# Optimization experiments

Hardware: AMD Instinct MI355X
Metric: run time of the kernel (lower is better)

## Reference

```python
import jax, jax.numpy as jnp
import numpy as np
from jax import lax

B, S, CIN, COUT, K = 32, 2048, 256, 256, 16


def setup_inputs() -> dict:
    key = jax.random.key(0)
    k1, k2, k3, k4 = jax.random.split(key, 4)
    x = jax.random.normal(k1, (B, S, CIN), dtype=jnp.float32)
    w_real = jax.random.normal(k2, (COUT, CIN, K), dtype=jnp.float32) * 0.1
    w_imag = jax.random.normal(k3, (COUT, CIN, K), dtype=jnp.float32) * 0.1
    phases = jax.random.normal(k4, (K,), dtype=jnp.float32) * 0.1
    return {"x": x, "w_real": w_real, "w_imag": w_imag, "phases": phases}


def reference(x, w_real, w_imag, phases):
    # out[b,t,o] = Re( sum_{k,i} x[b,t+k,i] * exp(1j*phases[k]) * (w_real + 1j*w_imag)[o,i,k] )
    # x is real, so this equals a real valid conv1d with effective kernel:
    #   w_eff[o,i,k] = cos(phases[k]) * w_real[o,i,k] - sin(phases[k]) * w_imag[o,i,k]
    w_eff = jnp.cos(phases)[None, None, :] * w_real - jnp.sin(phases)[None, None, :] * w_imag
    # conv expects NCH / OIH layouts
    y = lax.conv_general_dilated(
        jnp.transpose(x, (0, 2, 1)),  # [B, CIN, S]
        w_eff,                         # [COUT, CIN, K]
        window_strides=(1,),
        padding="VALID",
        dimension_numbers=("NCH", "OIH", "NCH"),
    )
    return jnp.transpose(y, (0, 2, 1))  # [B, S-K+1, COUT]
```

## Files before the change

### kernel.cpp

```cpp
#include <hip/hip_runtime.h>
#include <math.h>

#define B_    32
#define S_    2048
#define CIN_  256
#define COUT_ 256
#define K_    16
#define TOUT_ 2033
#define RTOT_ 4096

typedef __bf16 bf16x4 __attribute__((ext_vector_type(4)));
typedef __bf16 bf16x8 __attribute__((ext_vector_type(8)));
typedef float  f32x4  __attribute__((ext_vector_type(4)));

#define GLOBAL_AS __attribute__((address_space(1)))
#define LDS_AS    __attribute__((address_space(3)))

__device__ __forceinline__ void gload_lds16(const void* g, void* l) {
  __builtin_amdgcn_global_load_lds((const GLOBAL_AS void*)g, (LDS_AS void*)l, 16, 0, 0);
}

__global__ void __launch_bounds__(256) build_wt_kernel(const float* __restrict__ wr,
                                                       const float* __restrict__ wi,
                                                       const float* __restrict__ ph,
                                                       __bf16* __restrict__ wt) {
  int t = blockIdx.x * 256 + threadIdx.x;
  int o = t >> 8, i = t & 255;
  const float4* wr4 = (const float4*)(wr + (size_t)(o * CIN_ + i) * K_);
  const float4* wi4 = (const float4*)(wi + (size_t)(o * CIN_ + i) * K_);
  float re[16], im[16];
  #pragma unroll
  for (int v = 0; v < 4; v++) {
    float4 a = wr4[v];
    re[4*v+0]=a.x; re[4*v+1]=a.y; re[4*v+2]=a.z; re[4*v+3]=a.w;
    float4 b = wi4[v];
    im[4*v+0]=b.x; im[4*v+1]=b.y; im[4*v+2]=b.z; im[4*v+3]=b.w;
  }
  #pragma unroll
  for (int kk = 0; kk < K_; kk++) {
    float p = ph[kk];
    wt[(size_t)o * RTOT_ + kk * CIN_ + i] = (__bf16)(cosf(p)*re[kk] - sinf(p)*im[kk]);
  }
}

__global__ void __launch_bounds__(256, 4) conv_mfma_kernel(const float* __restrict__ xg,
                                                           const __bf16* __restrict__ wt,
                                                           float* __restrict__ out) {
  __shared__ __align__(16) __bf16 As[144 * 32];
  __shared__ __align__(16) __bf16 Bs[3][128 * 32];

  const int bx = blockIdx.x;
  const int nb = bx & 1;
  const int mb = (bx >> 1) & 15;
  const int b  = bx >> 5;

  const int tid  = threadIdx.x;
  const int w    = tid >> 6;
  const int lane = tid & 63;
  const int wm   = w >> 1, wn = w & 1;
  const int n16  = lane & 15, q = lane >> 4;

  const int t0 = mb * 128;
  const int o0 = nb * 128;

  const float* xbase = xg + (size_t)b * (S_ * CIN_);

  const int sr = tid >> 3;
  const int sc = (tid & 7) * 4;
  const int br = w * 16 + (lane >> 2);
  const int bc = (((lane & 3) ^ ((lane >> 3) & 3))) * 8;

  const int bswz = (n16 >> 1) & 3;

  f32x4 acc[4][4];
  #pragma unroll
  for (int im_ = 0; im_ < 4; im_++)
    #pragma unroll
    for (int in_ = 0; in_ < 4; in_++)
      acc[im_][in_] = {0.f, 0.f, 0.f, 0.f};

  auto stage_a = [&](int ic) {
    const float* xcol = xbase + ic * 32 + sc;
    #pragma unroll
    for (int p = 0; p < 4; p++) {
      int r = p * 32 + sr;
      int rg = t0 + r; rg = (rg < S_) ? rg : (S_ - 1);
      float4 v = *(const float4*)(xcol + (size_t)rg * CIN_);
      bf16x4 o4; o4[0]=(__bf16)v.x; o4[1]=(__bf16)v.y; o4[2]=(__bf16)v.z; o4[3]=(__bf16)v.w;
      *(bf16x4*)(As + r * 32 + (sc ^ (((r >> 1) & 3) << 3))) = o4;
    }
    if (tid < 128) {
      int r = 128 + sr;
      int rg = t0 + r; rg = (rg < S_) ? rg : (S_ - 1);
      float4 v = *(const float4*)(xcol + (size_t)rg * CIN_);
      bf16x4 o4; o4[0]=(__bf16)v.x; o4[1]=(__bf16)v.y; o4[2]=(__bf16)v.z; o4[3]=(__bf16)v.w;
      *(bf16x4*)(As + r * 32 + (sc ^ (((r >> 1) & 3) << 3))) = o4;
    }
  };

  auto stage_b = [&](int j, int buf) {
    const int kk = j & 15;
    const int i0 = (j >> 4) * 32;
    const __bf16* wcol = wt + (size_t)kk * CIN_ + i0 + bc;
    __bf16* dst = &Bs[0][0] + buf * (128 * 32) + (w * 16) * 32;
    #pragma unroll
    for (int p = 0; p < 2; p++) {
      int orow = o0 + p * 64 + br;
      gload_lds16(wcol + (size_t)orow * RTOT_, (void*)(dst + p * 64 * 32));
    }
  };

  stage_a(0);
  stage_b(0, 0);
  stage_b(1, 1);
  asm volatile("s_waitcnt vmcnt(2) lgkmcnt(0)\n\ts_barrier" ::: "memory");

  int jr = 0;
  int jw = 2;
  #pragma unroll 1
  for (int j = 0; j < 128; ++j) {
    const int kk = j & 15;

    if (j + 2 < 128) stage_b(j + 2, jw);

    const __bf16* bsr = &Bs[0][0] + jr * (128 * 32);
    const int aswz = ((kk + n16) >> 1) & 3;
    bf16x8 af[4], bfrag[4];
    #pragma unroll
    for (int jm = 0; jm < 4; jm++) {
      int row = kk + wm * 64 + jm * 16 + n16;
      af[jm] = *(const bf16x8*)(As + row * 32 + ((q ^ aswz) * 8));
    }
    #pragma unroll
    for (int jn = 0; jn < 4; jn++) {
      int row = wn * 64 + jn * 16 + n16;
      bfrag[jn] = *(const bf16x8*)(bsr + row * 32 + ((q ^ bswz) * 8));
    }

    __builtin_amdgcn_s_setprio(1);
    #pragma unroll
    for (int jm = 0; jm < 4; jm++)
      #pragma unroll
      for (int jn = 0; jn < 4; jn++)
        acc[jm][jn] = __builtin_amdgcn_mfma_f32_16x16x32_bf16(af[jm], bfrag[jn], acc[jm][jn], 0, 0, 0);
    __builtin_amdgcn_s_setprio(0);

    if (j == 127) break;

    if (j <= 125) asm volatile("s_waitcnt vmcnt(2)\n\ts_barrier" ::: "memory");
    else          asm volatile("s_waitcnt vmcnt(0)\n\ts_barrier" ::: "memory");

    if (kk == 15) {
      stage_a((j + 1) >> 4);
      asm volatile("s_waitcnt lgkmcnt(0)\n\ts_barrier" ::: "memory");
    }

    jr = (jr == 2) ? 0 : jr + 1;
    jw = (jw == 2) ? 0 : jw + 1;
  }

  float* obase = out + (size_t)b * TOUT_ * COUT_;
  #pragma unroll
  for (int jm = 0; jm < 4; jm++) {
    #pragma unroll
    for (int r = 0; r < 4; r++) {
      int t = t0 + wm * 64 + jm * 16 + q * 4 + r;
      if (t < TOUT_) {
        float* orow = obase + (size_t)t * COUT_ + o0 + wn * 64 + n16;
        #pragma unroll
        for (int jn = 0; jn < 4; jn++)
          orow[jn * 16] = acc[jm][jn][r];
      }
    }
  }
}

extern "C" void kernel_launch(void* const* d_in, const int* in_sizes, int n_in,
                              void* d_out, int out_size, void* d_ws, size_t ws_size,
                              hipStream_t stream) {
  const float* x  = (const float*)d_in[0];
  const float* wr = (const float*)d_in[1];
  const float* wi = (const float*)d_in[2];
  const float* ph = (const float*)d_in[3];
  float* out = (float*)d_out;

  __bf16* wt = (__bf16*)d_ws;

  build_wt_kernel<<<dim3((COUT_ * CIN_) / 256), dim3(256), 0, stream>>>(wr, wi, ph, wt);
  conv_mfma_kernel<<<dim3(B_ * 16 * 2), dim3(256), 0, stream>>>(x, wt, out);
}
```

Before: 220.6 us.

## Make weight tiles wave-local and prefetch MFMA fragments before the barrier

Each wave now stages with global_load_lds only the 64 weight rows of its own N half. The two waves that share a half issue duplicate, identical loads into the same LDS slots. Because of that, a wave can wait on its own vmcnt and read the next B fragments before the block barrier. The A fragments for the next k-offset are also read right after the MFMAs rather than at the top of the next iteration. The aim is to hide LDS read latency and shorten barrier stalls, at the cost of doubling weight load traffic, mostly served from cache, and using more registers for fragments held across iterations.

```diff
diff --git a/kernel.cpp b/kernel.cpp
--- a/kernel.cpp
+++ b/kernel.cpp
@@ -67,8 +67,8 @@
 
   const int sr = tid >> 3;
   const int sc = (tid & 7) * 4;
-  const int br = w * 16 + (lane >> 2);
-  const int bc = (((lane & 3) ^ ((lane >> 3) & 3))) * 8;
+  const int br2 = wn * 64 + (lane >> 2);
+  const int bc  = (((lane & 3) ^ ((lane >> 3) & 3))) * 8;
 
   const int bswz = (n16 >> 1) & 3;
 
@@ -102,40 +102,46 @@
     const int kk = j & 15;
     const int i0 = (j >> 4) * 32;
     const __bf16* wcol = wt + (size_t)kk * CIN_ + i0 + bc;
-    __bf16* dst = &Bs[0][0] + buf * (128 * 32) + (w * 16) * 32;
-    #pragma unroll
-    for (int p = 0; p < 2; p++) {
-      int orow = o0 + p * 64 + br;
-      gload_lds16(wcol + (size_t)orow * RTOT_, (void*)(dst + p * 64 * 32));
+    __bf16* dst = &Bs[0][0] + buf * (128 * 32) + (wn * 64) * 32;
+    #pragma unroll
+    for (int p = 0; p < 4; p++) {
+      int orow = o0 + br2 + p * 16;
+      gload_lds16(wcol + (size_t)orow * RTOT_, (void*)(dst + p * 16 * 32));
+    }
+  };
+
+  bf16x8 af[4], bfrag[4];
+  auto read_af = [&](int kp) {
+    const int aswz = ((kp + n16) >> 1) & 3;
+    #pragma unroll
+    for (int jm = 0; jm < 4; jm++) {
+      int row = kp + wm * 64 + jm * 16 + n16;
+      af[jm] = *(const bf16x8*)(As + row * 32 + ((q ^ aswz) * 8));
+    }
+  };
+  auto read_bf = [&](int buf) {
+    const __bf16* bsr = &Bs[0][0] + buf * (128 * 32);
+    #pragma unroll
+    for (int jn = 0; jn < 4; jn++) {
+      int row = wn * 64 + jn * 16 + n16;
+      bfrag[jn] = *(const bf16x8*)(bsr + row * 32 + ((q ^ bswz) * 8));
     }
   };
 
   stage_a(0);
   stage_b(0, 0);
   stage_b(1, 1);
-  asm volatile("s_waitcnt vmcnt(2) lgkmcnt(0)\n\ts_barrier" ::: "memory");
-
-  int jr = 0;
-  int jw = 2;
+  asm volatile("s_waitcnt vmcnt(4) lgkmcnt(0)\n\ts_barrier" ::: "memory");
+  read_af(0);
+  read_bf(0);
+
+  int sw = 2;
+  int fr = 1;
   #pragma unroll 1
   for (int j = 0; j < 128; ++j) {
     const int kk = j & 15;
 
-    if (j + 2 < 128) stage_b(j + 2, jw);
-
-    const __bf16* bsr = &Bs[0][0] + jr * (128 * 32);
-    const int aswz = ((kk + n16) >> 1) & 3;
-    bf16x8 af[4], bfrag[4];
-    #pragma unroll
-    for (int jm = 0; jm < 4; jm++) {
-      int row = kk + wm * 64 + jm * 16 + n16;
-      af[jm] = *(const bf16x8*)(As + row * 32 + ((q ^ aswz) * 8));
-    }
-    #pragma unroll
-    for (int jn = 0; jn < 4; jn++) {
-      int row = wn * 64 + jn * 16 + n16;
-      bfrag[jn] = *(const bf16x8*)(bsr + row * 32 + ((q ^ bswz) * 8));
-    }
+    if (j + 2 < 128) stage_b(j + 2, sw);
 
     __builtin_amdgcn_s_setprio(1);
     #pragma unroll
@@ -147,16 +153,23 @@
 
     if (j == 127) break;
 
-    if (j <= 125) asm volatile("s_waitcnt vmcnt(2)\n\ts_barrier" ::: "memory");
-    else          asm volatile("s_waitcnt vmcnt(0)\n\ts_barrier" ::: "memory");
-
-    if (kk == 15) {
+    const bool bdry = (kk == 15);
+    if (!bdry) read_af(kk + 1);
+
+    if (j <= 125) asm volatile("s_waitcnt vmcnt(4)" ::: "memory");
+    else          asm volatile("s_waitcnt vmcnt(0)" ::: "memory");
+    read_bf(fr);
+
+    asm volatile("s_barrier" ::: "memory");
+
+    if (bdry) {
       stage_a((j + 1) >> 4);
       asm volatile("s_waitcnt lgkmcnt(0)\n\ts_barrier" ::: "memory");
-    }
-
-    jr = (jr == 2) ? 0 : jr + 1;
-    jw = (jw == 2) ? 0 : jw + 1;
+      read_af(0);
+    }
+
+    sw = (sw == 2) ? 0 : sw + 1;
+    fr = (fr == 2) ? 0 : fr + 1;
   }
 
   float* obase = out + (size_t)b * TOUT_ * COUT_;
```

Measured after the change: 251.9 us. +14.2%, slower.

## Reorder weight reduction axis and prefetch LDS fragments with deeper B pipeline

Applied to the files above, without the earlier changes.

The weight build kernel now writes a different reduction ordering, where each 32-wide chunk interleaves two taps over 16 input channels. The A tile shrinks to 16 channels and is restaged every 8 iterations instead of 16. The B ring buffer grows from 3 to 4 stages, and the A and B fragments for the next iteration are read from LDS before the barrier so those reads overlap with the MFMAs. This aims to hide LDS and global latency and cut LDS footprint, at the cost of more frequent A restaging and more complex swizzle indexing.

```diff
diff --git a/kernel.cpp b/kernel.cpp
--- a/kernel.cpp
+++ b/kernel.cpp
@@ -36,18 +36,19 @@
     float4 b = wi4[v];
     im[4*v+0]=b.x; im[4*v+1]=b.y; im[4*v+2]=b.z; im[4*v+3]=b.w;
   }
+  __bf16* wrow = wt + (size_t)o * RTOT_ + (i >> 4) * 256 + (i & 15);
   #pragma unroll
-  for (int kk = 0; kk < K_; kk++) {
-    float p = ph[kk];
-    wt[(size_t)o * RTOT_ + kk * CIN_ + i] = (__bf16)(cosf(p)*re[kk] - sinf(p)*im[kk]);
+  for (int k = 0; k < K_; k++) {
+    float p = ph[k];
+    wrow[(k >> 1) * 32 + ((k & 1) << 4)] = (__bf16)(cosf(p)*re[k] - sinf(p)*im[k]);
   }
 }
 
 __global__ void __launch_bounds__(256, 4) conv_mfma_kernel(const float* __restrict__ xg,
                                                            const __bf16* __restrict__ wt,
                                                            float* __restrict__ out) {
-  __shared__ __align__(16) __bf16 As[144 * 32];
-  __shared__ __align__(16) __bf16 Bs[3][128 * 32];
+  __shared__ __align__(16) __bf16 As[144 * 16];
+  __shared__ __align__(16) __bf16 Bs[4][128 * 32];
 
   const int bx = blockIdx.x;
   const int nb = bx & 1;
@@ -65,11 +66,8 @@
 
   const float* xbase = xg + (size_t)b * (S_ * CIN_);
 
-  const int sr = tid >> 3;
-  const int sc = (tid & 7) * 4;
   const int br = w * 16 + (lane >> 2);
-  const int bc = (((lane & 3) ^ ((lane >> 3) & 3))) * 8;
-
+  const int bc = ((lane & 3) ^ ((lane >> 3) & 3)) * 8;
   const int bswz = (n16 >> 1) & 3;
 
   f32x4 acc[4][4];
@@ -79,29 +77,25 @@
     for (int in_ = 0; in_ < 4; in_++)
       acc[im_][in_] = {0.f, 0.f, 0.f, 0.f};
 
-  auto stage_a = [&](int ic) {
-    const float* xcol = xbase + ic * 32 + sc;
+  auto stage_a = [&](int g) {
+    const int i0 = g * 16;
     #pragma unroll
-    for (int p = 0; p < 4; p++) {
-      int r = p * 32 + sr;
-      int rg = t0 + r; rg = (rg < S_) ? rg : (S_ - 1);
-      float4 v = *(const float4*)(xcol + (size_t)rg * CIN_);
-      bf16x4 o4; o4[0]=(__bf16)v.x; o4[1]=(__bf16)v.y; o4[2]=(__bf16)v.z; o4[3]=(__bf16)v.w;
-      *(bf16x4*)(As + r * 32 + (sc ^ (((r >> 1) & 3) << 3))) = o4;
-    }
-    if (tid < 128) {
-      int r = 128 + sr;
-      int rg = t0 + r; rg = (rg < S_) ? rg : (S_ - 1);
-      float4 v = *(const float4*)(xcol + (size_t)rg * CIN_);
-      bf16x4 o4; o4[0]=(__bf16)v.x; o4[1]=(__bf16)v.y; o4[2]=(__bf16)v.z; o4[3]=(__bf16)v.w;
-      *(bf16x4*)(As + r * 32 + (sc ^ (((r >> 1) & 3) << 3))) = o4;
+    for (int p = 0; p < 3; p++) {
+      int c = tid + p * 256;
+      if (c < 572) {
+        int r = c >> 2, sc = (c & 3) * 4;
+        int rg = t0 + r; rg = (rg < S_) ? rg : (S_ - 1);
+        float4 v = *(const float4*)(xbase + (size_t)rg * CIN_ + i0 + sc);
+        bf16x4 o4; o4[0]=(__bf16)v.x; o4[1]=(__bf16)v.y; o4[2]=(__bf16)v.z; o4[3]=(__bf16)v.w;
+        int byte = r * 32 + sc * 2;
+        byte ^= ((r >> 3) & 7) << 4;
+        *(bf16x4*)((char*)As + byte) = o4;
+      }
     }
   };
 
-  auto stage_b = [&](int j, int buf) {
-    const int kk = j & 15;
-    const int i0 = (j >> 4) * 32;
-    const __bf16* wcol = wt + (size_t)kk * CIN_ + i0 + bc;
+  auto stage_b = [&](int jj, int buf) {
+    const __bf16* wcol = wt + (size_t)jj * 32 + bc;
     __bf16* dst = &Bs[0][0] + buf * (128 * 32) + (w * 16) * 32;
     #pragma unroll
     for (int p = 0; p < 2; p++) {
@@ -110,32 +104,33 @@
     }
   };
 
-  stage_a(0);
-  stage_b(0, 0);
-  stage_b(1, 1);
-  asm volatile("s_waitcnt vmcnt(2) lgkmcnt(0)\n\ts_barrier" ::: "memory");
-
-  int jr = 0;
-  int jw = 2;
-  #pragma unroll 1
-  for (int j = 0; j < 128; ++j) {
-    const int kk = j & 15;
-
-    if (j + 2 < 128) stage_b(j + 2, jw);
-
-    const __bf16* bsr = &Bs[0][0] + jr * (128 * 32);
-    const int aswz = ((kk + n16) >> 1) & 3;
-    bf16x8 af[4], bfrag[4];
+  bf16x8 af[4], bfrag[4];
+  auto read_af = [&](int tp) {
     #pragma unroll
     for (int jm = 0; jm < 4; jm++) {
-      int row = kk + wm * 64 + jm * 16 + n16;
-      af[jm] = *(const bf16x8*)(As + row * 32 + ((q ^ aswz) * 8));
+      int r = 2 * tp + wm * 64 + jm * 16 + n16 + (q >> 1);
+      int byte = (r * 32 + (q & 1) * 16) ^ (((r >> 3) & 7) << 4);
+      af[jm] = *(const bf16x8*)((const char*)As + byte);
     }
+  };
+  auto read_bf = [&](int buf) {
+    const __bf16* bsr = &Bs[0][0] + buf * (128 * 32);
     #pragma unroll
     for (int jn = 0; jn < 4; jn++) {
       int row = wn * 64 + jn * 16 + n16;
       bfrag[jn] = *(const bf16x8*)(bsr + row * 32 + ((q ^ bswz) * 8));
     }
+  };
+
+  stage_a(0);
+  stage_b(0, 0); stage_b(1, 1); stage_b(2, 2);
+  asm volatile("s_waitcnt vmcnt(2) lgkmcnt(0)\n\ts_barrier" ::: "memory");
+  read_af(0);
+  read_bf(0);
+
+  #pragma unroll 1
+  for (int j = 0; j < 128; ++j) {
+    if (j + 3 < 128) stage_b(j + 3, (j + 3) & 3);
 
     __builtin_amdgcn_s_setprio(1);
     #pragma unroll
@@ -146,17 +141,20 @@
     __builtin_amdgcn_s_setprio(0);
 
     if (j == 127) break;
+    const bool bdry = ((j & 7) == 7);
 
-    if (j <= 125) asm volatile("s_waitcnt vmcnt(2)\n\ts_barrier" ::: "memory");
-    else          asm volatile("s_waitcnt vmcnt(0)\n\ts_barrier" ::: "memory");
+    if (!bdry) read_af((j + 1) & 7);
 
-    if (kk == 15) {
-      stage_a((j + 1) >> 4);
+    if (j <= 124) asm volatile("s_waitcnt vmcnt(2)" ::: "memory");
+    else          asm volatile("s_waitcnt vmcnt(0)" ::: "memory");
+    read_bf((j + 1) & 3);
+    asm volatile("s_barrier" ::: "memory");
+
+    if (bdry) {
+      stage_a((j >> 3) + 1);
       asm volatile("s_waitcnt lgkmcnt(0)\n\ts_barrier" ::: "memory");
+      read_af(0);
     }
-
-    jr = (jr == 2) ? 0 : jr + 1;
-    jw = (jw == 2) ? 0 : jw + 1;
   }
 
   float* obase = out + (size_t)b * TOUT_ * COUT_;
```

Measured after the change: 233.5 us. +5.8%, slower.

## Load weight fragments directly from global into registers, drop LDS B staging

Applied to the files above, without the earlier changes.

The weight prepack kernel now writes weights in a fragment-friendly tiled layout, so each lane can load its MFMA B operands straight from global memory (L2-resident) into registers. The triple-buffered LDS B staging and the per-iteration barriers are removed and replaced by register double-buffering over two k-steps. Barriers remain only around the A-tile restage. This trades LDS traffic and synchronisation for extra global/L2 loads per wave and depends on load latency being hidden by the MFMA cluster.

```diff
diff --git a/kernel.cpp b/kernel.cpp
--- a/kernel.cpp
+++ b/kernel.cpp
@@ -7,18 +7,10 @@
 #define COUT_ 256
 #define K_    16
 #define TOUT_ 2033
-#define RTOT_ 4096
 
 typedef __bf16 bf16x4 __attribute__((ext_vector_type(4)));
 typedef __bf16 bf16x8 __attribute__((ext_vector_type(8)));
 typedef float  f32x4  __attribute__((ext_vector_type(4)));
-
-#define GLOBAL_AS __attribute__((address_space(1)))
-#define LDS_AS    __attribute__((address_space(3)))
-
-__device__ __forceinline__ void gload_lds16(const void* g, void* l) {
-  __builtin_amdgcn_global_load_lds((const GLOBAL_AS void*)g, (LDS_AS void*)l, 16, 0, 0);
-}
 
 __global__ void __launch_bounds__(256) build_wt_kernel(const float* __restrict__ wr,
                                                        const float* __restrict__ wi,
@@ -36,10 +28,13 @@
     float4 b = wi4[v];
     im[4*v+0]=b.x; im[4*v+1]=b.y; im[4*v+2]=b.z; im[4*v+3]=b.w;
   }
+  const int nb = o >> 7, r = o & 127, ic = i >> 5, e = i & 31;
+  __bf16* base = wt + (size_t)nb * (128 * 128 * 32)
+                    + (size_t)(ic * 16) * 4096 + r * 32 + e;
   #pragma unroll
-  for (int kk = 0; kk < K_; kk++) {
-    float p = ph[kk];
-    wt[(size_t)o * RTOT_ + kk * CIN_ + i] = (__bf16)(cosf(p)*re[kk] - sinf(p)*im[kk]);
+  for (int k = 0; k < K_; k++) {
+    float p = ph[k];
+    base[(size_t)k * 4096] = (__bf16)(cosf(p)*re[k] - sinf(p)*im[k]);
   }
 }
 
@@ -47,7 +42,6 @@
                                                            const __bf16* __restrict__ wt,
                                                            float* __restrict__ out) {
   __shared__ __align__(16) __bf16 As[144 * 32];
-  __shared__ __align__(16) __bf16 Bs[3][128 * 32];
 
   const int bx = blockIdx.x;
   const int nb = bx & 1;
@@ -67,10 +61,9 @@
 
   const int sr = tid >> 3;
   const int sc = (tid & 7) * 4;
-  const int br = w * 16 + (lane >> 2);
-  const int bc = (((lane & 3) ^ ((lane >> 3) & 3))) * 8;
 
-  const int bswz = (n16 >> 1) & 3;
+  const char* bb = (const char*)(wt + (size_t)nb * (128 * 128 * 32))
+                 + ((wn * 64 + n16) * 32 + q * 8) * 2;
 
   f32x4 acc[4][4];
   #pragma unroll
@@ -98,66 +91,56 @@
     }
   };
 
-  auto stage_b = [&](int j, int buf) {
-    const int kk = j & 15;
-    const int i0 = (j >> 4) * 32;
-    const __bf16* wcol = wt + (size_t)kk * CIN_ + i0 + bc;
-    __bf16* dst = &Bs[0][0] + buf * (128 * 32) + (w * 16) * 32;
+  bf16x8 af[4], bf0[4], bf1[4];
+
+  auto read_af = [&](int kp) {
+    const int aswz = ((kp + n16) >> 1) & 3;
     #pragma unroll
-    for (int p = 0; p < 2; p++) {
-      int orow = o0 + p * 64 + br;
-      gload_lds16(wcol + (size_t)orow * RTOT_, (void*)(dst + p * 64 * 32));
+    for (int jm = 0; jm < 4; jm++) {
+      int row = kp + wm * 64 + jm * 16 + n16;
+      af[jm] = *(const bf16x8*)(As + row * 32 + ((q ^ aswz) * 8));
     }
   };
+  auto load_b = [&](bf16x8* dst, int j) {
+    const char* p = bb + (size_t)j * 8192;
+    #pragma unroll
+    for (int jn = 0; jn < 4; jn++)
+      dst[jn] = *(const bf16x8*)(p + jn * 1024);
+  };
+
+  #define MFMA_CLUSTER(BF)                                                        \
+    __builtin_amdgcn_s_setprio(1);                                                \
+    _Pragma("unroll")                                                             \
+    for (int jm = 0; jm < 4; jm++)                                                \
+      _Pragma("unroll")                                                           \
+      for (int jn = 0; jn < 4; jn++)                                              \
+        acc[jm][jn] = __builtin_amdgcn_mfma_f32_16x16x32_bf16(af[jm], (BF)[jn],   \
+                                                              acc[jm][jn], 0, 0, 0); \
+    __builtin_amdgcn_s_setprio(0);
 
   stage_a(0);
-  stage_b(0, 0);
-  stage_b(1, 1);
-  asm volatile("s_waitcnt vmcnt(2) lgkmcnt(0)\n\ts_barrier" ::: "memory");
+  load_b(bf0, 0);
+  asm volatile("s_waitcnt lgkmcnt(0)\n\ts_barrier" ::: "memory");
 
-  int jr = 0;
-  int jw = 2;
   #pragma unroll 1
-  for (int j = 0; j < 128; ++j) {
+  for (int j = 0; j < 128; j += 2) {
     const int kk = j & 15;
 
-    if (j + 2 < 128) stage_b(j + 2, jw);
+    load_b(bf1, j + 1);
+    read_af(kk);
+    MFMA_CLUSTER(bf0);
 
-    const __bf16* bsr = &Bs[0][0] + jr * (128 * 32);
-    const int aswz = ((kk + n16) >> 1) & 3;
-    bf16x8 af[4], bfrag[4];
-    #pragma unroll
-    for (int jm = 0; jm < 4; jm++) {
-      int row = kk + wm * 64 + jm * 16 + n16;
-      af[jm] = *(const bf16x8*)(As + row * 32 + ((q ^ aswz) * 8));
-    }
-    #pragma unroll
-    for (int jn = 0; jn < 4; jn++) {
-      int row = wn * 64 + jn * 16 + n16;
-      bfrag[jn] = *(const bf16x8*)(bsr + row * 32 + ((q ^ bswz) * 8));
-    }
+    if (j + 2 < 128) load_b(bf0, j + 2);
+    read_af(kk + 1);
+    MFMA_CLUSTER(bf1);
 
-    __builtin_amdgcn_s_setprio(1);
-    #pragma unroll
-    for (int jm = 0; jm < 4; jm++)
-      #pragma unroll
-      for (int jn = 0; jn < 4; jn++)
-        acc[jm][jn] = __builtin_amdgcn_mfma_f32_16x16x32_bf16(af[jm], bfrag[jn], acc[jm][jn], 0, 0, 0);
-    __builtin_amdgcn_s_setprio(0);
-
-    if (j == 127) break;
-
-    if (j <= 125) asm volatile("s_waitcnt vmcnt(2)\n\ts_barrier" ::: "memory");
-    else          asm volatile("s_waitcnt vmcnt(0)\n\ts_barrier" ::: "memory");
-
-    if (kk == 15) {
-      stage_a((j + 1) >> 4);
+    if (kk == 14 && j + 2 < 128) {
+      asm volatile("s_barrier" ::: "memory");
+      stage_a((j >> 4) + 1);
       asm volatile("s_waitcnt lgkmcnt(0)\n\ts_barrier" ::: "memory");
     }
-
-    jr = (jr == 2) ? 0 : jr + 1;
-    jw = (jw == 2) ? 0 : jw + 1;
   }
+  #undef MFMA_CLUSTER
 
   float* obase = out + (size_t)b * TOUT_ * COUT_;
   #pragma unroll
```

After: 254.3 us. +15.3%, slower.
